# Kernel optimization log

Measured on AMD Instinct MI355X. Metric: run time of the kernel, lower is better.

The kernel has to match this reference:

```python
import jax, jax.numpy as jnp
import numpy as np

THR = 0.05          # init kwarg thr
MARGIN = 1.0        # torch TripletMarginLoss default used in module
PD_EPS = 1e-6       # torch pairwise_distance eps (added to the difference)
NORM_EPS = 1e-12    # torch F.normalize eps


def _l2_normalize(X):
    n = jnp.linalg.norm(X, axis=1, keepdims=True)
    return X / jnp.maximum(n, NORM_EPS)


def _pdist(Xn):
    # D[i,j] = || Xn[i] - Xn[j] + eps ||_2, computed without an NxNxd tensor:
    # ||a-b+e||^2 = ||a||^2 + ||b||^2 - 2 a.b + 2e*(sum(a)-sum(b)) + d*e^2
    d = Xn.shape[1]
    s2 = jnp.sum(Xn * Xn, axis=1)
    G = Xn @ Xn.T
    rs = jnp.sum(Xn, axis=1)
    D2 = (s2[:, None] + s2[None, :] - 2.0 * G
          + 2.0 * PD_EPS * (rs[:, None] - rs[None, :]) + d * (PD_EPS ** 2))
    return jnp.sqrt(jnp.maximum(D2, 0.0))


def _forward(Xs):
    # 1) per-view thresholded similarity graphs
    graphs = []
    for X in Xs:
        Xn = _l2_normalize(X)
        S = Xn @ Xn.T
        graphs.append((S > THR).astype(X.dtype))
    # 2) Despite in-place aliasing in the torch code, each view's effective
    #    adjacency is the clipped union of all view graphs minus the diagonal.
    U = jnp.minimum(sum(graphs), 1.0)
    N = U.shape[0]
    A = U - jnp.eye(N, dtype=U.dtype)
    pos_mask = A > 0                      # anchors/positives
    zero_mask = (A == 0)                  # negative candidates (incl. self, as in torch)
    csum = jnp.cumsum(zero_mask.astype(jnp.int32), axis=1)  # [N,N] per-row zero ranks
    cnt = csum[:, -1]                     # negatives per row (>0 w.h.p.)
    key = jax.random.key(42)

    def row_search(c, r):                 # first k with csum[k] > r -> rank-r zero
        return jnp.searchsorted(c, r, side='right')

    total = jnp.asarray(0.0, dtype=Xs[0].dtype)
    for v, X in enumerate(Xs):
        Xn = _l2_normalize(X)
        D = _pdist(Xn)                    # [N,N] anchor-to-all distances
        u = jax.random.uniform(jax.random.fold_in(key, v), (N, N), dtype=jnp.float32)
        r = jnp.minimum((u * cnt[:, None].astype(jnp.float32)).astype(jnp.int32),
                        jnp.maximum(cnt[:, None] - 1, 0))
        n_idx = jax.vmap(row_search)(csum, r)              # [N,N] sampled negative per (i,p)
        d_an = jnp.take_along_axis(D, n_idx, axis=1)
        loss_pair = jnp.maximum(D - d_an + MARGIN, 0.0)    # d(a,p) - d(a,n) + margin
        m = pos_mask.astype(X.dtype)
        total = total + jnp.sum(loss_pair * m) / jnp.sum(m)
    return total


def setup_inputs() -> dict:
    key = jax.random.key(0)
    k0, k1, k2 = jax.random.split(key, 3)
    N, d = 4096, 512
    return {
        "X0": jax.random.normal(k0, (N, d), dtype=jnp.float32),
        "X1": jax.random.normal(k1, (N, d), dtype=jnp.float32),
        "X2": jax.random.normal(k2, (N, d), dtype=jnp.float32),
    }


def reference(X0, X1, X2):
    return _forward([X0, X1, X2])
```

## Files before the change

### kernel.cpp

```cpp
#include <hip/hip_runtime.h>
#include <stdint.h>

#define NROW 4096
#define NDIM 512
#define THRS 0.05f

typedef __attribute__((ext_vector_type(8))) __bf16 bf16x8;
typedef __attribute__((ext_vector_type(4))) float f32x4;

#define XHI_OFF  0ull
#define XHI_SZ   (3ull*4096ull*512ull*2ull)
#define XLO_OFF  (XHI_OFF + XHI_SZ)
#define XLO_SZ   XHI_SZ
#define RT_OFF   (XLO_OFF + XLO_SZ)
#define RT_SZ    (3ull*4096ull*4ull)
#define CT_OFF   (RT_OFF + RT_SZ)
#define CT_SZ    (3ull*4096ull*4ull)
#define G_OFF    (CT_OFF + CT_SZ)
#define G_SZ     (3ull*4096ull*4096ull*4ull)
#define ACC_OFF  (G_OFF + G_SZ)
#define WS_NEEDED (ACC_OFF + 64ull)

__host__ __device__ __forceinline__ void tf2x32(uint32_t k0, uint32_t k1,
                                                uint32_t x0, uint32_t x1,
                                                uint32_t* o0, uint32_t* o1) {
  uint32_t ks2 = k0 ^ k1 ^ 0x1BD11BDAu;
  x0 += k0; x1 += k1;
#define TFR(r) { x0 += x1; x1 = (x1 << (r)) | (x1 >> (32 - (r))); x1 ^= x0; }
  TFR(13) TFR(15) TFR(26) TFR(6)
  x0 += k1; x1 += ks2 + 1u;
  TFR(17) TFR(29) TFR(16) TFR(24)
  x0 += ks2; x1 += k0 + 2u;
  TFR(13) TFR(15) TFR(26) TFR(6)
  x0 += k0; x1 += k1 + 3u;
  TFR(17) TFR(29) TFR(16) TFR(24)
  x0 += k1; x1 += ks2 + 4u;
  TFR(13) TFR(15) TFR(26) TFR(6)
  x0 += ks2; x1 += k0 + 5u;
#undef TFR
  *o0 = x0; *o1 = x1;
}

struct Keys { uint32_t k[6]; };

__global__ __launch_bounds__(128) void norm_kernel(const float* __restrict__ X,
                                                   __bf16* __restrict__ Xhi,
                                                   __bf16* __restrict__ Xlo,
                                                   float* __restrict__ rowT,
                                                   float* __restrict__ colT) {
  const int row = blockIdx.x;
  const int tid = threadIdx.x;
  const int lane = tid & 63, wid = tid >> 6;
  const float4 v = *(const float4*)(X + (size_t)row * NDIM + tid * 4);
  float ss = v.x*v.x + v.y*v.y + v.z*v.z + v.w*v.w;
  #pragma unroll
  for (int off = 32; off; off >>= 1) ss += __shfl_down(ss, off);
  __shared__ float sw[2];
  if (lane == 0) sw[wid] = ss;
  __syncthreads();
  const float tot = sw[0] + sw[1];
  const float den = fmaxf(sqrtf(tot), 1e-12f);
  float n[4];
  n[0] = v.x / den; n[1] = v.y / den; n[2] = v.z / den; n[3] = v.w / den;

  __bf16 hi[4], lo[4];
  #pragma unroll
  for (int e = 0; e < 4; ++e) {
    hi[e] = (__bf16)n[e];
    lo[e] = (__bf16)(n[e] - (float)hi[e]);
  }
  *(ushort4*)(Xhi + (size_t)row * NDIM + tid * 4) = *(ushort4*)hi;
  *(ushort4*)(Xlo + (size_t)row * NDIM + tid * 4) = *(ushort4*)lo;

  float ps = n[0] + n[1] + n[2] + n[3];
  float p2 = n[0]*n[0] + n[1]*n[1] + n[2]*n[2] + n[3]*n[3];
  #pragma unroll
  for (int off = 32; off; off >>= 1) { ps += __shfl_down(ps, off); p2 += __shfl_down(p2, off); }
  __shared__ float sw2[4];
  if (lane == 0) { sw2[wid] = ps; sw2[2 + wid] = p2; }
  __syncthreads();
  if (tid == 0) {
    const float rs = sw2[0] + sw2[1];
    const float s2 = sw2[2] + sw2[3];
    rowT[row] = s2 + 2e-6f * rs + 5.12e-10f;
    colT[row] = s2 - 2e-6f * rs;
  }
}

__global__ __launch_bounds__(256) void gemm_syrk_bf16(const __bf16* __restrict__ XhiBase,
                                                      const __bf16* __restrict__ XloBase,
                                                      float* __restrict__ CBase) {
  const int bx = blockIdx.x;
  const int v = bx / 528;
  const int t = bx - v * 528;
  int bi = (int)((65.0f - sqrtf(4225.0f - 8.0f * (float)t)) * 0.5f);
  while ((bi + 1) * (65 - (bi + 1)) / 2 <= t) ++bi;
  while (bi * (65 - bi) / 2 > t) --bi;
  const int bj = bi + (t - bi * (65 - bi) / 2);

  const __bf16* __restrict__ Ahi = XhiBase + (size_t)v * NROW * NDIM;
  const __bf16* __restrict__ Alo = XloBase + (size_t)v * NROW * NDIM;
  float* __restrict__ C = CBase + ((size_t)v << 24);

  __shared__ __bf16 As[128][64];
  __shared__ __bf16 Bs[128][64];
  const int tid = threadIdx.x;
  const int lane = tid & 63;
  const int wid = tid >> 6;
  const int wr = wid >> 1, wc = wid & 1;

  f32x4 zero4 = {0.f, 0.f, 0.f, 0.f};
  f32x4 acc[4][4];
  #pragma unroll
  for (int m = 0; m < 4; ++m)
    #pragma unroll
    for (int n = 0; n < 4; ++n) acc[m][n] = zero4;

  const int lrow = lane >> 3;
  const int lcol = (lane & 7) * 8;
  const int fr = lane & 15;
  const int fk = (lane >> 4) * 8;

  for (int kt = 0; kt < 1536; kt += 64) {
    const int s = kt >> 9;
    const int colk = kt & 511;
    const __bf16* __restrict__ Asrc = (s < 2) ? Ahi : Alo;
    const __bf16* __restrict__ Bsrc = (s == 1) ? Alo : Ahi;
    #pragma unroll
    for (int p = 0; p < 4; ++p) {
      const int c = wid * 4 + p;
      const int trow = c * 8 + lrow;
      const __bf16* ga = Asrc + (((size_t)(bi * 128 + trow)) << 9) + colk + lcol;
      const __bf16* gb = Bsrc + (((size_t)(bj * 128 + trow)) << 9) + colk + lcol;
      __builtin_amdgcn_global_load_lds((const __attribute__((address_space(1))) void*)ga,
                                       (__attribute__((address_space(3))) void*)((char*)&As[0][0] + c * 1024),
                                       16, 0, 0);
      __builtin_amdgcn_global_load_lds((const __attribute__((address_space(1))) void*)gb,
                                       (__attribute__((address_space(3))) void*)((char*)&Bs[0][0] + c * 1024),
                                       16, 0, 0);
    }
    __syncthreads();
    #pragma unroll
    for (int kk = 0; kk < 64; kk += 32) {
      bf16x8 af[4], bfr[4];
      #pragma unroll
      for (int m = 0; m < 4; ++m)
        af[m] = *(const bf16x8*)&As[wr * 64 + m * 16 + fr][kk + fk];
      #pragma unroll
      for (int n = 0; n < 4; ++n)
        bfr[n] = *(const bf16x8*)&Bs[wc * 64 + n * 16 + fr][kk + fk];
      #pragma unroll
      for (int m = 0; m < 4; ++m)
        #pragma unroll
        for (int n = 0; n < 4; ++n)
          acc[m][n] = __builtin_amdgcn_mfma_f32_16x16x32_bf16(af[m], bfr[n], acc[m][n], 0, 0, 0);
    }
    __syncthreads();
  }

  const int cl = lane & 15;
  const int rg = (lane >> 4) * 4;
  #pragma unroll
  for (int m = 0; m < 4; ++m) {
    #pragma unroll
    for (int n = 0; n < 4; ++n) {
      const int r0 = bi * 128 + wr * 64 + m * 16 + rg;
      const int c0 = bj * 128 + wc * 64 + n * 16 + cl;
      #pragma unroll
      for (int q = 0; q < 4; ++q)
        C[(size_t)(r0 + q) * NROW + c0] = acc[m][n][q];
      if (bi != bj) {
        #pragma unroll
        for (int q = 0; q < 4; ++q)
          C[(size_t)c0 * NROW + (r0 + q)] = acc[m][n][q];
      }
    }
  }
}

__global__ __launch_bounds__(256, 4) void loss_kernel(const float* __restrict__ G,
                                                      const float* __restrict__ rowT,
                                                      const float* __restrict__ colT,
                                                      double* __restrict__ lossAcc,
                                                      unsigned long long* __restrict__ posAcc,
                                                      Keys keys) {
  __shared__ float sBuf[NROW];
  __shared__ unsigned short zlist[NROW];
  __shared__ unsigned short plist[NROW];
  __shared__ unsigned char nib[1024];
  __shared__ int sWaveTot[4];
  __shared__ float sLoss[4];

  const int i = blockIdx.x;
  const int tid = threadIdx.x;
  const int lane = tid & 63, wid = tid >> 6;

  {
    bool posb[4][4];
    #pragma unroll
    for (int p = 0; p < 4; ++p) {
      const int j4 = p * 1024 + tid * 4;
      #pragma unroll
      for (int e = 0; e < 4; ++e) posb[p][e] = false;
      #pragma unroll
      for (int v = 0; v < 3; ++v) {
        const float4 g = *(const float4*)(G + ((size_t)v << 24) + ((size_t)i << 12) + j4);
        posb[p][0] |= (g.x > THRS); posb[p][1] |= (g.y > THRS);
        posb[p][2] |= (g.z > THRS); posb[p][3] |= (g.w > THRS);
      }
      unsigned int z = 0;
      #pragma unroll
      for (int e = 0; e < 4; ++e) {
        const int j = j4 + e;
        const bool pos = posb[p][e] && (j != i);
        if (!pos) z |= (1u << e);
      }
      nib[p * 256 + tid] = (unsigned char)z;
    }
  }
  __syncthreads();

  const uchar4 myn = *(const uchar4*)&nib[tid * 4];
  const int cz = __popc((unsigned)myn.x) + __popc((unsigned)myn.y) +
                 __popc((unsigned)myn.z) + __popc((unsigned)myn.w);
  int inc = cz;
  #pragma unroll
  for (int off = 1; off < 64; off <<= 1) {
    const int s = __shfl_up(inc, off);
    if (lane >= off) inc += s;
  }
  if (lane == 63) sWaveTot[wid] = inc;
  __syncthreads();
  int base = inc - cz;
  for (int w = 0; w < wid; ++w) base += sWaveTot[w];
  const int cnt = sWaveTot[0] + sWaveTot[1] + sWaveTot[2] + sWaveTot[3];
  {
    int zr = base;
    const unsigned char nn[4] = { myn.x, myn.y, myn.z, myn.w };
    #pragma unroll
    for (int q = 0; q < 4; ++q) {
      const int jb = tid * 16 + q * 4;
      #pragma unroll
      for (int e = 0; e < 4; ++e) {
        const int j = jb + e;
        if ((nn[q] >> e) & 1) { zlist[zr] = (unsigned short)j; ++zr; }
        else                  { plist[j - zr] = (unsigned short)j; }
      }
    }
  }
  __syncthreads();

  const int npos = NROW - cnt;
  const float cntf = (float)cnt;
  const int cm1 = cnt - 1;
  float lossSum = 0.0f;

  #pragma unroll
  for (int v = 0; v < 3; ++v) {
    const float rT = rowT[v * NROW + i];
    const float* __restrict__ cT = colT + v * NROW;
    const float* __restrict__ g = G + ((size_t)v << 24) + ((size_t)i << 12);
    #pragma unroll
    for (int p = 0; p < 4; ++p) {
      const int j4 = p * 1024 + tid * 4;
      const float4 gg = *(const float4*)(g + j4);
      const float4 ct = *(const float4*)(cT + j4);
      float4 d;
      d.x = sqrtf(fmaxf((rT + ct.x) - 2.0f * gg.x, 0.0f));
      d.y = sqrtf(fmaxf((rT + ct.y) - 2.0f * gg.y, 0.0f));
      d.z = sqrtf(fmaxf((rT + ct.z) - 2.0f * gg.z, 0.0f));
      d.w = sqrtf(fmaxf((rT + ct.w) - 2.0f * gg.w, 0.0f));
      *(float4*)&sBuf[j4] = d;
    }
    __syncthreads();

    const uint32_t fk0 = keys.k[2 * v], fk1 = keys.k[2 * v + 1];
    const uint32_t tbase = (uint32_t)i * 4096u;
    for (int k = tid; k < npos; k += 256) {
      const int j = plist[k];
      const uint32_t t32 = tbase + (uint32_t)j;
      uint32_t y0, y1, bits;
      if (i < 2048) { tf2x32(fk0, fk1, t32, t32 + 8388608u, &y0, &y1); bits = y0; }
      else          { tf2x32(fk0, fk1, t32 - 8388608u, t32, &y0, &y1); bits = y1; }
      const float u = __uint_as_float((bits >> 9) | 0x3F800000u) - 1.0f;
      int r = (int)(u * cntf);
      r = min(r, cm1);
      const int n = zlist[r];
      lossSum += fmaxf(sBuf[j] - sBuf[n] + 1.0f, 0.0f);
    }
    __syncthreads();
  }

  #pragma unroll
  for (int off = 32; off; off >>= 1) lossSum += __shfl_down(lossSum, off);
  if (lane == 0) sLoss[wid] = lossSum;
  __syncthreads();
  if (tid == 0) {
    const double tot = (double)sLoss[0] + (double)sLoss[1] + (double)sLoss[2] + (double)sLoss[3];
    atomicAdd(lossAcc, tot);
    atomicAdd(posAcc, (unsigned long long)npos);
  }
}

__global__ void finalize_kernel(const double* __restrict__ lossAcc,
                                const unsigned long long* __restrict__ posAcc,
                                float* __restrict__ out) {
  if (threadIdx.x == 0 && blockIdx.x == 0) {
    out[0] = (float)(lossAcc[0] / (double)posAcc[0]);
  }
}

extern "C" void kernel_launch(void* const* d_in, const int* in_sizes, int n_in,
                              void* d_out, int out_size, void* d_ws, size_t ws_size,
                              hipStream_t stream) {
  if (ws_size < WS_NEEDED) return;

  const float* Xs[3] = { (const float*)d_in[0], (const float*)d_in[1], (const float*)d_in[2] };
  char* ws = (char*)d_ws;
  __bf16* Xhi = (__bf16*)(ws + XHI_OFF);
  __bf16* Xlo = (__bf16*)(ws + XLO_OFF);
  float* rowT = (float*)(ws + RT_OFF);
  float* colT = (float*)(ws + CT_OFF);
  float* G  = (float*)(ws + G_OFF);
  double* lossAcc = (double*)(ws + ACC_OFF);
  unsigned long long* posAcc = (unsigned long long*)(ws + ACC_OFF + 8);
  float* out = (float*)d_out;

  hipMemsetAsync(ws + ACC_OFF, 0, 16, stream);

  for (int v = 0; v < 3; ++v)
    norm_kernel<<<NROW, 128, 0, stream>>>(Xs[v],
                                          Xhi + (size_t)v * NROW * NDIM,
                                          Xlo + (size_t)v * NROW * NDIM,
                                          rowT + v * NROW, colT + v * NROW);

  gemm_syrk_bf16<<<3 * 528, 256, 0, stream>>>(Xhi, Xlo, G);

  Keys keys;
  for (uint32_t v = 0; v < 3; ++v) {
    uint32_t y0, y1;
    tf2x32(0u, 42u, 0u, v, &y0, &y1);
    keys.k[2 * v] = y0; keys.k[2 * v + 1] = y1;
  }

  loss_kernel<<<NROW, 256, 0, stream>>>(G, rowT, colT, lossAcc, posAcc, keys);
  finalize_kernel<<<1, 1, 0, stream>>>(lossAcc, posAcc, out);
}
```

Baseline: 363.6 us.

## Stage GEMM epilogue through LDS for coalesced float4 stores and remap block order

The SYRK GEMM epilogue now stages accumulator tiles through reused shared memory in two halves, for both the direct and transposed tile. Each tile is then written to global memory with coalesced float4 stores instead of scattered scalar stores, which matters most for the strided transposed writes. Block indices are also remapped by interleaving in groups of eight, likely to spread work across XCDs or improve cache locality. The cost is extra barriers and LDS traffic in the epilogue, plus a larger shared allocation.

New measurement: 359.1 us. Within noise of the previous version (-1.2%).

```diff
diff --git a/kernel.cpp b/kernel.cpp
--- a/kernel.cpp
+++ b/kernel.cpp
@@ -90,7 +90,9 @@
 __global__ __launch_bounds__(256) void gemm_syrk_bf16(const __bf16* __restrict__ XhiBase,
                                                       const __bf16* __restrict__ XloBase,
                                                       float* __restrict__ CBase) {
-  const int bx = blockIdx.x;
+  const int orig = blockIdx.x;
+  const int bx = (orig & 7) * (1584 >> 3) + (orig >> 3);
+
   const int v = bx / 528;
   const int t = bx - v * 528;
   int bi = (int)((65.0f - sqrtf(4225.0f - 8.0f * (float)t)) * 0.5f);
@@ -102,8 +104,10 @@
   const __bf16* __restrict__ Alo = XloBase + (size_t)v * NROW * NDIM;
   float* __restrict__ C = CBase + ((size_t)v << 24);
 
-  __shared__ __bf16 As[128][64];
-  __shared__ __bf16 Bs[128][64];
+  __shared__ __align__(16) char smemRaw[34816];
+  __bf16 (*As)[64] = (__bf16 (*)[64])smemRaw;
+  __bf16 (*Bs)[64] = (__bf16 (*)[64])(smemRaw + 16384);
+
   const int tid = threadIdx.x;
   const int lane = tid & 63;
   const int wid = tid >> 6;
@@ -133,10 +137,10 @@
       const __bf16* ga = Asrc + (((size_t)(bi * 128 + trow)) << 9) + colk + lcol;
       const __bf16* gb = Bsrc + (((size_t)(bj * 128 + trow)) << 9) + colk + lcol;
       __builtin_amdgcn_global_load_lds((const __attribute__((address_space(1))) void*)ga,
-                                       (__attribute__((address_space(3))) void*)((char*)&As[0][0] + c * 1024),
+                                       (__attribute__((address_space(3))) void*)(smemRaw + c * 1024),
                                        16, 0, 0);
       __builtin_amdgcn_global_load_lds((const __attribute__((address_space(1))) void*)gb,
-                                       (__attribute__((address_space(3))) void*)((char*)&Bs[0][0] + c * 1024),
+                                       (__attribute__((address_space(3))) void*)(smemRaw + 16384 + c * 1024),
                                        16, 0, 0);
     }
     __syncthreads();
@@ -160,19 +164,48 @@
 
   const int cl = lane & 15;
   const int rg = (lane >> 4) * 4;
-  #pragma unroll
-  for (int m = 0; m < 4; ++m) {
-    #pragma unroll
-    for (int n = 0; n < 4; ++n) {
-      const int r0 = bi * 128 + wr * 64 + m * 16 + rg;
-      const int c0 = bj * 128 + wc * 64 + n * 16 + cl;
-      #pragma unroll
-      for (int q = 0; q < 4; ++q)
-        C[(size_t)(r0 + q) * NROW + c0] = acc[m][n][q];
-      if (bi != bj) {
+  float (*Ls)[136] = (float (*)[136])smemRaw;
+  float (*Lt)[68]  = (float (*)[68])smemRaw;
+
+  __syncthreads();
+  #pragma unroll
+  for (int r = 0; r < 2; ++r) {
+    if (r) __syncthreads();
+    if (wr == r) {
+      #pragma unroll
+      for (int m = 0; m < 4; ++m)
         #pragma unroll
-        for (int q = 0; q < 4; ++q)
-          C[(size_t)c0 * NROW + (r0 + q)] = acc[m][n][q];
+        for (int n = 0; n < 4; ++n)
+          #pragma unroll
+          for (int q = 0; q < 4; ++q)
+            Ls[m * 16 + rg + q][wc * 64 + n * 16 + cl] = acc[m][n][q];
+    }
+    __syncthreads();
+    #pragma unroll
+    for (int q = 0; q < 8; ++q) {
+      const int idx = q * 256 + tid;
+      const int row = idx >> 5, c4 = idx & 31;
+      *(float4*)&C[(size_t)(bi * 128 + r * 64 + row) * NROW + bj * 128 + c4 * 4] =
+          *(const float4*)&Ls[row][c4 * 4];
+    }
+    if (bi != bj) {
+      __syncthreads();
+      if (wr == r) {
+        #pragma unroll
+        for (int m = 0; m < 4; ++m)
+          #pragma unroll
+          for (int n = 0; n < 4; ++n)
+            #pragma unroll
+            for (int q = 0; q < 4; ++q)
+              Lt[wc * 64 + n * 16 + cl][m * 16 + rg + q] = acc[m][n][q];
+      }
+      __syncthreads();
+      #pragma unroll
+      for (int q = 0; q < 8; ++q) {
+        const int idx = q * 256 + tid;
+        const int mrow = idx >> 4, c4 = idx & 15;
+        *(float4*)&C[(size_t)(bj * 128 + mrow) * NROW + bi * 128 + r * 64 + c4 * 4] =
+            *(const float4*)&Lt[mrow][c4 * 4];
       }
     }
   }
```
